# Kernel tuning notes

Hardware: AMD Instinct MI355X
Metric: run time of the kernel (lower is better)

## Reference

```python
import jax, jax.numpy as jnp
import numpy as np

EPS = 0.2        # epsilon from init_kwargs
MIN_POINTS = 10  # minPoints from init_kwargs

def setup_inputs() -> dict:
    key = jax.random.key(0)
    points = jax.random.normal(key, (16384, 3), dtype=jnp.float32)
    return {"points": points}

def _dbscan(points):
    # Faithful DBSCAN semantics of the torch module: brute-force region query
    # (dist < eps, self included since d(p,p)=0<eps), core if |neighbors| >= minPoints,
    # clusters = connected components of the eps-graph restricted to core points,
    # border points join the lowest-scan-order cluster among their core neighbors
    # (matches the sequential scan-order cluster numbering), everything else -1.
    N = points.shape[0]
    sq = jnp.sum(points * points, axis=1)                       # [N]
    # ||xi - xj||^2 via GEMM expansion (avoids the [N,N,3] diff tensor)
    d2 = sq[:, None] + sq[None, :] - 2.0 * (points @ points.T)  # [N,N]
    adj = d2 < (EPS * EPS)                                      # strict <, as in torch code
    deg = jnp.sum(adj, axis=1)
    core = deg >= MIN_POINTS                                    # [N] bool
    core_adj = adj & core[:, None] & core[None, :]              # core<->core edges

    BIG = N  # sentinel label larger than any point index
    idx = jnp.arange(N)
    lab0 = jnp.where(core, idx, BIG)

    # min-label propagation until fixed point => component root = min core index,
    # which equals the first core point of that cluster in scan order.
    def cond(state):
        _, changed = state
        return changed

    def body(state):
        lab, _ = state
        nb = jnp.min(jnp.where(core_adj, lab[None, :], BIG), axis=1)
        new = jnp.minimum(lab, nb)
        return (new, jnp.any(new != lab))

    lab, _ = jax.lax.while_loop(cond, body, (lab0, jnp.array(True)))

    # every point's root = min root among its core neighbors (core points include self)
    root = jnp.min(jnp.where(adj & core[None, :], lab[None, :], BIG), axis=1)
    reached = root < BIG  # core or border; otherwise noise

    # renumber roots to sequential cluster ids in scan order
    is_root = core & (lab == idx)
    rank = jnp.cumsum(is_root.astype(jnp.int32)) - 1            # cluster id at each root index
    cid = rank[jnp.minimum(root, N - 1)]
    labels = jnp.where(reached, cid, -1).astype(jnp.float32)
    return labels.reshape(-1, 1)

def reference(points):
    return _dbscan(points)
```

## Files before the change

### kernel.cpp

```cpp
#include <hip/hip_runtime.h>
#include <stdint.h>


#define N_PTS   16384
#define BLOCK   256
#define EPS2    0.04f
#define G       32
#define GCELLS  (G * G * G)
#define GLO     -4.5f
#define GSCALE  3.5555556f
#define NRANGE  27
#define EBLK    (NRANGE * N_PTS / BLOCK)
#define LBUF    4096
#define LB1     2048
#define ECAP    262144
#define MCAP    65536
#define SCAP    131072
#define BCAP    131072
#define HSIZE   32768
#define NCC     1024
#define CHUNK   (N_PTS / NCC)
#define BIG     N_PTS
#define ENCB    16400
#define HUGEV   (1 << 29)
#define HEMPTY  0xFFFFFFFFu


__device__ __forceinline__ float sqsum(float x, float y, float z) {
    return __fadd_rn(__fadd_rn(__fmul_rn(x, x), __fmul_rn(y, y)), __fmul_rn(z, z));
}
__device__ __forceinline__ float dist2(float px, float py, float pz, float sqi, float4 q) {
    float dot = __fmaf_rn(pz, q.z, __fmaf_rn(py, q.y, __fmul_rn(px, q.x)));
    return __fsub_rn(__fadd_rn(sqi, q.w), __fmul_rn(2.0f, dot));
}
__device__ __forceinline__ int pload(const int* p) {
    return __hip_atomic_load(p, __ATOMIC_RELAXED, __HIP_MEMORY_SCOPE_AGENT);
}
__device__ __forceinline__ uint32_t uload(const uint32_t* p) {
    return __hip_atomic_load(p, __ATOMIC_RELAXED, __HIP_MEMORY_SCOPE_AGENT);
}
__device__ __forceinline__ int cellco(float v) {
    int c = (int)floorf(__fmul_rn(__fsub_rn(v, GLO), GSCALE));
    return min(max(c, 0), G - 1);
}

__global__ void k_hist(const float* __restrict__ pts, uint32_t* __restrict__ cnts,
                       int* __restrict__ parent, uint32_t* __restrict__ htab,
                       uint32_t* __restrict__ hcnt, uint32_t* __restrict__ cellof) {
    const int p = blockIdx.x * BLOCK + threadIdx.x;
    if (blockIdx.x == 0 && threadIdx.x < 3) cnts[2 + threadIdx.x] = 0;
    parent[p] = p;
    htab[p] = HEMPTY; htab[p + N_PTS] = HEMPTY;
    float x = pts[3 * p], y = pts[3 * p + 1], z = pts[3 * p + 2];
    uint32_t c = (uint32_t)((cellco(z) * G + cellco(y)) * G + cellco(x));
    cellof[p] = c;
    atomicAdd(&hcnt[c], 1u);
}

__global__ void __launch_bounds__(1024)
k_scan(const uint32_t* __restrict__ hcnt, const uint32_t* __restrict__ cnts,
       uint32_t* __restrict__ cellstart, uint32_t* __restrict__ cursor) {
    __shared__ uint32_t wsum[16];
    const int tid = threadIdx.x, lane = tid & 63, wv = tid >> 6;
    const uint32_t B = cnts[15];
    uint32_t loc[32];
#pragma unroll
    for (int k = 0; k < 8; ++k) {
        uint4 v = ((const uint4*)hcnt)[tid * 8 + k];
        loc[4 * k + 0] = v.x - B; loc[4 * k + 1] = v.y - B;
        loc[4 * k + 2] = v.z - B; loc[4 * k + 3] = v.w - B;
    }
    uint32_t tot = 0;
#pragma unroll
    for (int k = 0; k < 32; ++k) tot += loc[k];
    uint32_t incl = tot;
#pragma unroll
    for (int d = 1; d < 64; d <<= 1) { uint32_t t2 = __shfl_up(incl, d, 64); if (lane >= d) incl += t2; }
    if (lane == 63) wsum[wv] = incl;
    __syncthreads();
    uint32_t wbase = 0;
    for (int w = 0; w < wv; ++w) wbase += wsum[w];
    uint32_t off = wbase + incl - tot;
#pragma unroll
    for (int k = 0; k < 32; ++k) {
        uint32_t c = (uint32_t)tid * 32u + (uint32_t)k;
        cellstart[c] = off; cursor[c] = off;
        off += loc[k];
    }
    if (tid == 1023) cellstart[GCELLS] = off;
}

__global__ void k_scatter(const float* __restrict__ pts, const uint32_t* __restrict__ cellof,
                          uint32_t* __restrict__ cursor, float4* __restrict__ spts,
                          int* __restrict__ sid) {
    const int p = blockIdx.x * BLOCK + threadIdx.x;
    uint32_t c = cellof[p];
    uint32_t pos = atomicAdd(&cursor[c], 1u);
    float x = pts[3 * p], y = pts[3 * p + 1], z = pts[3 * p + 2];
    spts[pos] = make_float4(x, y, z, sqsum(x, y, z));
    sid[pos] = p;
}

__global__ void k_edges_b(const float4* __restrict__ spts, const int* __restrict__ sid,
                          const uint32_t* __restrict__ cellstart,
                          uint32_t* __restrict__ edges, uint32_t* __restrict__ cnts,
                          uint32_t* __restrict__ deg) {
    const uint32_t B = cnts[15];
    const int tid = threadIdx.x;
    __shared__ uint32_t lbuf[LBUF];
    __shared__ uint32_t lcnt, lbase;
    if (tid == 0) lcnt = 0;
    __syncthreads();
    const int r = blockIdx.x >> 6;
    const int p = ((blockIdx.x & 63) << 8) + tid;
    float4 me = spts[p];
    const int ig = sid[p];
    const int cx = cellco(me.x), cy = cellco(me.y), cz = cellco(me.z);
    const int x = cx + (r % 3) - 1;
    const int y = cy + ((r / 3) % 3) - 1;
    const int z = cz + (r / 9) - 1;
    uint32_t cnt = 0;
    if ((unsigned)x < (unsigned)G && (unsigned)y < (unsigned)G && (unsigned)z < (unsigned)G) {
        const int c = (z * G + y) * G + x;
        uint32_t q = cellstart[c];
        const uint32_t qe = cellstart[c + 1];
        for (; q < qe; ++q) {
            float4 o = spts[q];
            float d2 = dist2(me.x, me.y, me.z, me.w, o);
            if (d2 < EPS2) {
                ++cnt;
                int jg = sid[q];
                if (jg < ig) {
                    uint32_t s = atomicAdd(&lcnt, 1u);
                    uint32_t pk = ((uint32_t)ig << 14) | (uint32_t)jg;
                    if (s < LBUF) lbuf[s] = pk;
                    else {
                        uint32_t pos = atomicAdd(&cnts[1], 1u) - B;
                        if (pos < ECAP) edges[pos] = pk;
                    }
                }
            }
        }
    }
    if (cnt) atomicAdd(&deg[ig], cnt);
    __syncthreads();
    if (tid == 0) {
        uint32_t n = min(lcnt, (uint32_t)LBUF);
        lcnt = n;
        lbase = atomicAdd(&cnts[1], n) - B;
    }
    __syncthreads();
    for (uint32_t t2 = tid; t2 < lcnt; t2 += BLOCK) {
        uint32_t s2 = lbase + t2;
        if (s2 < ECAP) edges[s2] = lbuf[t2];
    }
}

__global__ void k_hook0(const uint32_t* __restrict__ edges, uint32_t* __restrict__ cnts,
                        const uint32_t* __restrict__ deg, int* __restrict__ parent,
                        uint32_t* __restrict__ mbuf) {
    const uint32_t B = cnts[15];
    const int n = min((int)(uload(&cnts[1]) - B), ECAP);
    const int lane = threadIdx.x & 63;
    const uint64_t lane_lt = (1ull << lane) - 1;
    for (int e = blockIdx.x * BLOCK + threadIdx.x; e < n; e += gridDim.x * BLOCK) {
        uint32_t p = edges[e];
        int i = (int)(p >> 14), j = (int)(p & (N_PTS - 1));
        bool ci = (deg[i] - B) >= 10u;
        bool cj = (deg[j] - B) >= 10u;
        if (ci && cj) atomicMin(&parent[max(i, j)], min(i, j));
        bool mx = ci != cj;
        uint64_t m2 = __ballot(mx);
        if (m2) {
            int ldr = (int)__ffsll((unsigned long long)m2) - 1;
            uint32_t base = 0;
            if (lane == ldr) base = atomicAdd(&cnts[3], (uint32_t)__popcll(m2));
            base = __shfl(base, ldr);
            if (mx) {
                uint32_t pk = ci ? (((uint32_t)i << 14) | (uint32_t)j)
                                 : (((uint32_t)j << 14) | (uint32_t)i);
                uint32_t pos = base + (uint32_t)__popcll(m2 & lane_lt);
                if (pos < MCAP) mbuf[pos] = pk;
            }
        }
    }
}

__global__ void k_jump(int* __restrict__ parent) {
    int x = blockIdx.x * BLOCK + threadIdx.x;
    int p = pload(&parent[x]);
    if (p == x) return;
    int r = p;
    while (true) { int q = pload(&parent[r]); if (q == r) break; r = q; }
    if (r != p)
        __hip_atomic_store(&parent[x], r, __ATOMIC_RELAXED, __HIP_MEMORY_SCOPE_AGENT);
}

__global__ void k_hook1(const uint32_t* __restrict__ edges, uint32_t* __restrict__ cnts,
                        const uint32_t* __restrict__ deg, int* __restrict__ parent,
                        uint32_t* __restrict__ surv, uint32_t* __restrict__ htab) {
    const uint32_t B = cnts[15];
    const int n = min((int)(uload(&cnts[1]) - B), ECAP);
    const int tid = threadIdx.x;
    __shared__ uint32_t lbuf[LB1];
    __shared__ uint32_t lcnt, lbase;
    if (tid == 0) lcnt = 0;
    __syncthreads();
    for (int e = blockIdx.x * BLOCK + tid; e < n; e += gridDim.x * BLOCK) {
        uint32_t p = edges[e];
        int i = (int)(p >> 14), j = (int)(p & (N_PTS - 1));
        bool cc = ((deg[i] - B) >= 10u) && ((deg[j] - B) >= 10u);
        if (cc) {
            int ri = pload(&parent[i]);
            int rj = pload(&parent[j]);
            if (ri != rj) {
                int lo = min(ri, rj), hi = max(ri, rj);
                uint32_t pk = ((uint32_t)hi << 14) | (uint32_t)lo;
                uint32_t h = (pk * 2654435761u) >> 17;
                if (atomicExch(&htab[h], pk) != pk) {
                    atomicMin(&parent[hi], lo);
                    uint32_t s = atomicAdd(&lcnt, 1u);
                    if (s < LB1) lbuf[s] = pk;
                    else {
                        uint32_t pos = atomicAdd(&cnts[4], 1u);
                        if (pos < SCAP) surv[pos] = pk;
                    }
                }
            }
        }
    }
    __syncthreads();
    if (tid == 0) {
        uint32_t n2 = min(lcnt, (uint32_t)LB1);
        lcnt = n2;
        lbase = atomicAdd(&cnts[4], n2);
    }
    __syncthreads();
    for (uint32_t t2 = tid; t2 < lcnt; t2 += BLOCK) {
        uint32_t s2 = lbase + t2;
        if (s2 < SCAP) surv[s2] = lbuf[t2];
    }
}

__global__ void __launch_bounds__(NCC)
k_cc_final(const int* __restrict__ parent_g, const uint32_t* __restrict__ deg,
           const uint32_t* __restrict__ surv, uint32_t* __restrict__ cnts,
           const uint32_t* __restrict__ mbuf,
           uint32_t* __restrict__ bufA, uint32_t* __restrict__ bufB,
           float* __restrict__ out) {
    __shared__ int lpar[N_PTS];
    __shared__ int s_nout;
    __shared__ int wsum[16];
    const int tid = threadIdx.x, lane = tid & 63, wv = tid >> 6;
    const uint64_t lane_lt = (1ull << lane) - 1;
    const uint32_t B = cnts[15];

#pragma unroll
    for (int k = 0; k < CHUNK; ++k) {
        int x = k * NCC + tid;
        lpar[x] = ((deg[x] - B) >= 10u) ? pload(&parent_g[x]) : BIG;
    }
    __syncthreads();
    {
        int v[CHUNK];
#pragma unroll
        for (int k = 0; k < CHUNK; ++k) v[k] = lpar[k * NCC + tid];
        bool any = true;
        while (any) {
            any = false;
#pragma unroll
            for (int k = 0; k < CHUNK; ++k) {
                if (v[k] < BIG) {
                    int q = lpar[v[k]];
                    if (q != v[k]) { v[k] = q; any = true; }
                }
            }
        }
#pragma unroll
        for (int k = 0; k < CHUNK; ++k)
            if (v[k] < BIG) lpar[k * NCC + tid] = v[k];
    }
    __syncthreads();

    int n_in = min((int)uload(&cnts[4]), SCAP);
    const uint32_t* cur = surv;
    for (int r = 0; r < 24; ++r) {
        uint32_t* nxt = (r & 1) ? bufB : bufA;
        if (tid == 0) s_nout = 0;
        __syncthreads();
        const int n4 = (n_in + 3) & ~3;
        for (int bb = tid * 4; bb < n4; bb += NCC * 4) {
            uint4 pk4 = *(const uint4*)(cur + bb);
#pragma unroll
            for (int k = 0; k < 4; ++k) {
                uint32_t p = (k == 0) ? pk4.x : (k == 1) ? pk4.y : (k == 2) ? pk4.z : pk4.w;
                bool valid = (bb + k) < n_in;
                int ri = 0, rj = 0;
                if (valid) {
                    ri = lpar[(int)(p >> 14)];
                    rj = lpar[(int)(p & (N_PTS - 1))];
                }
                bool live = valid && (ri != rj);
                int lo = min(ri, rj), hi = max(ri, rj);
                if (live) atomicMin(&lpar[hi], lo);
                uint64_t m = __ballot(live);
                if (m) {
                    int ldr = (int)__ffsll((unsigned long long)m) - 1;
                    int base = 0;
                    if (lane == ldr) base = atomicAdd(&s_nout, (int)__popcll(m));
                    base = __shfl(base, ldr);
                    if (live) {
                        int pos = base + (int)__popcll(m & lane_lt);
                        if (pos < BCAP) nxt[pos] = ((uint32_t)hi << 14) | (uint32_t)lo;
                    }
                }
            }
        }
        __syncthreads();
        if (s_nout == 0) break;
        int v[CHUNK];
#pragma unroll
        for (int k = 0; k < CHUNK; ++k) v[k] = lpar[k * NCC + tid];
        bool any = true;
        while (any) {
            any = false;
#pragma unroll
            for (int k = 0; k < CHUNK; ++k) {
                if (v[k] < BIG) {
                    int q = lpar[v[k]];
                    if (q != v[k]) { v[k] = q; any = true; }
                }
            }
        }
#pragma unroll
        for (int k = 0; k < CHUNK; ++k)
            if (v[k] < BIG) lpar[k * NCC + tid] = v[k];
        n_in = min(s_nout, BCAP);
        cur = nxt;
    }

    const int bn = tid * CHUNK;
    int fl[CHUNK]; int s = 0;
#pragma unroll
    for (int k = 0; k < CHUNK; ++k) {
        fl[k] = (lpar[bn + k] == bn + k) ? 1 : 0;
        s += fl[k];
    }
    int incl = s;
#pragma unroll
    for (int d = 1; d < 64; d <<= 1) { int t = __shfl_up(incl, d, 64); if (lane >= d) incl += t; }
    if (lane == 63) wsum[wv] = incl;
    __syncthreads();
    int wbase = 0;
    for (int w = 0; w < wv; ++w) wbase += wsum[w];
    int c = wbase + incl - s;
#pragma unroll
    for (int k = 0; k < CHUNK; ++k)
        if (fl[k]) lpar[bn + k] = ENCB + (c++);
    __syncthreads();
#pragma unroll
    for (int k = 0; k < CHUNK; ++k) {
        int x = k * NCC + tid;
        int p = lpar[x];
        if (p < BIG) lpar[x] = lpar[p];
        else if (p == BIG) lpar[x] = HUGEV;
    }
    __syncthreads();
    int nm = min((int)uload(&cnts[3]), MCAP);
    const int nm4 = (nm + 3) & ~3;
    for (int bb = tid * 4; bb < nm4; bb += NCC * 4) {
        uint4 p4 = *(const uint4*)(mbuf + bb);
#pragma unroll
        for (int k = 0; k < 4; ++k) {
            if (bb + k < nm) {
                uint32_t p = (k == 0) ? p4.x : (k == 1) ? p4.y : (k == 2) ? p4.z : p4.w;
                int cc = (int)(p >> 14), bb2 = (int)(p & (N_PTS - 1));
                atomicMin(&lpar[bb2], lpar[cc]);
            }
        }
    }
    __syncthreads();
#pragma unroll
    for (int k = 0; k < CHUNK; ++k) {
        int x = k * NCC + tid;
        int v = lpar[x];
        out[x] = (v < HUGEV) ? (float)(v - ENCB) : -1.0f;
    }
}

extern "C" void kernel_launch(void* const* d_in, const int* in_sizes, int n_in,
                              void* d_out, int out_size, void* d_ws, size_t ws_size,
                              hipStream_t stream) {
    (void)in_sizes; (void)n_in; (void)out_size; (void)ws_size;
    const float* pts = (const float*)d_in[0];
    float* out = (float*)d_out;

    uint32_t* ub = (uint32_t*)d_ws;
    uint32_t* deg       = ub;
    int*      parent    = (int*)(ub + 16384);
    uint32_t* cnts      = ub + 32768;
    uint32_t* edges     = ub + 32832;
    uint32_t* mbuf      = ub + 294976;
    uint32_t* surv      = ub + 360512;
    uint32_t* bufA      = ub + 491584;
    uint32_t* bufB      = ub + 622656;
    uint32_t* htab      = ub + 753728;
    uint32_t* hcnt      = ub + 786496;
    uint32_t* cellstart = ub + 819264;
    uint32_t* cursor    = ub + 852048;
    uint32_t* cellof    = ub + 884816;
    int*      sid       = (int*)(ub + 901200);
    float4*   spts      = (float4*)(ub + 917584);

    dim3 blk(BLOCK);
    k_hist    <<<dim3(N_PTS / BLOCK), blk, 0, stream>>>(pts, cnts, parent, htab, hcnt, cellof);
    k_scan    <<<dim3(1), dim3(1024), 0, stream>>>(hcnt, cnts, cellstart, cursor);
    k_scatter <<<dim3(N_PTS / BLOCK), blk, 0, stream>>>(pts, cellof, cursor, spts, sid);
    k_edges_b <<<dim3(EBLK), blk, 0, stream>>>(spts, sid, cellstart, edges, cnts, deg);
    k_hook0   <<<dim3(1024), blk, 0, stream>>>(edges, cnts, deg, parent, mbuf);
    k_jump    <<<dim3(N_PTS / BLOCK), blk, 0, stream>>>(parent);
    k_hook1   <<<dim3(512), blk, 0, stream>>>(edges, cnts, deg, parent, surv, htab);
    k_cc_final<<<dim3(1), dim3(NCC), 0, stream>>>(parent, deg, surv, cnts,
                                                  mbuf, bufA, bufB, out);
}
```

Baseline: 157.6 us.

## Use half-neighbourhood cell stencil and symmetric edge emission in edge kernel

The edge-building kernel now scans only 13 forward neighbour cells plus the later points of its own cell, instead of all 27 cells. Each pair is tested once, both endpoints' degrees are incremented through an atomic on the partner, and a canonically ordered edge is emitted. Because self-pairs are no longer counted, the core threshold drops from 10 to 9. This roughly halves the distance tests, at the cost of extra global atomics on deg and more shared-buffer appends per block.

```diff
diff --git a/kernel.cpp b/kernel.cpp
--- a/kernel.cpp
+++ b/kernel.cpp
@@ -9,7 +9,7 @@
 #define GCELLS  (G * G * G)
 #define GLO     -4.5f
 #define GSCALE  3.5555556f
-#define NRANGE  27
+#define NRANGE  14
 #define EBLK    (NRANGE * N_PTS / BLOCK)
 #define LBUF    4096
 #define LB1     2048
@@ -116,28 +116,43 @@
     float4 me = spts[p];
     const int ig = sid[p];
     const int cx = cellco(me.x), cy = cellco(me.y), cz = cellco(me.z);
-    const int x = cx + (r % 3) - 1;
-    const int y = cy + ((r / 3) % 3) - 1;
-    const int z = cz + (r / 9) - 1;
+    uint32_t q = 0, qe = 0;
+    bool run = true;
+    if (r == 13) {
+        const int c = (cz * G + cy) * G + cx;
+        q = (uint32_t)p + 1u;
+        qe = cellstart[c + 1];
+        run = q < qe;
+    } else {
+        int dx, dy, dz;
+        if (r < 9)       { dz = 1; dy = r / 3 - 1; dx = r % 3 - 1; }
+        else if (r < 12) { dz = 0; dy = 1;         dx = r - 10;    }
+        else             { dz = 0; dy = 0;         dx = 1;         }
+        const int x = cx + dx, y = cy + dy, z = cz + dz;
+        run = (unsigned)x < (unsigned)G && (unsigned)y < (unsigned)G && (unsigned)z < (unsigned)G;
+        if (run) {
+            const int c = (z * G + y) * G + x;
+            q = cellstart[c];
+            qe = cellstart[c + 1];
+            run = q < qe;
+        }
+    }
     uint32_t cnt = 0;
-    if ((unsigned)x < (unsigned)G && (unsigned)y < (unsigned)G && (unsigned)z < (unsigned)G) {
-        const int c = (z * G + y) * G + x;
-        uint32_t q = cellstart[c];
-        const uint32_t qe = cellstart[c + 1];
+    if (run) {
         for (; q < qe; ++q) {
             float4 o = spts[q];
             float d2 = dist2(me.x, me.y, me.z, me.w, o);
             if (d2 < EPS2) {
                 ++cnt;
                 int jg = sid[q];
-                if (jg < ig) {
-                    uint32_t s = atomicAdd(&lcnt, 1u);
-                    uint32_t pk = ((uint32_t)ig << 14) | (uint32_t)jg;
-                    if (s < LBUF) lbuf[s] = pk;
-                    else {
-                        uint32_t pos = atomicAdd(&cnts[1], 1u) - B;
-                        if (pos < ECAP) edges[pos] = pk;
-                    }
+                atomicAdd(&deg[jg], 1u);
+                uint32_t pk = ig > jg ? (((uint32_t)ig << 14) | (uint32_t)jg)
+                                      : (((uint32_t)jg << 14) | (uint32_t)ig);
+                uint32_t s = atomicAdd(&lcnt, 1u);
+                if (s < LBUF) lbuf[s] = pk;
+                else {
+                    uint32_t pos = atomicAdd(&cnts[1], 1u) - B;
+                    if (pos < ECAP) edges[pos] = pk;
                 }
             }
         }
@@ -166,8 +181,8 @@
     for (int e = blockIdx.x * BLOCK + threadIdx.x; e < n; e += gridDim.x * BLOCK) {
         uint32_t p = edges[e];
         int i = (int)(p >> 14), j = (int)(p & (N_PTS - 1));
-        bool ci = (deg[i] - B) >= 10u;
-        bool cj = (deg[j] - B) >= 10u;
+        bool ci = (deg[i] - B) >= 9u;
+        bool cj = (deg[j] - B) >= 9u;
         if (ci && cj) atomicMin(&parent[max(i, j)], min(i, j));
         bool mx = ci != cj;
         uint64_t m2 = __ballot(mx);
@@ -209,7 +224,7 @@
     for (int e = blockIdx.x * BLOCK + tid; e < n; e += gridDim.x * BLOCK) {
         uint32_t p = edges[e];
         int i = (int)(p >> 14), j = (int)(p & (N_PTS - 1));
-        bool cc = ((deg[i] - B) >= 10u) && ((deg[j] - B) >= 10u);
+        bool cc = ((deg[i] - B) >= 9u) && ((deg[j] - B) >= 9u);
         if (cc) {
             int ri = pload(&parent[i]);
             int rj = pload(&parent[j]);
@@ -258,7 +273,7 @@
 #pragma unroll
     for (int k = 0; k < CHUNK; ++k) {
         int x = k * NCC + tid;
-        lpar[x] = ((deg[x] - B) >= 10u) ? pload(&parent_g[x]) : BIG;
+        lpar[x] = ((deg[x] - B) >= 9u) ? pload(&parent_g[x]) : BIG;
     }
     __syncthreads();
     {
```

After: 154.2 us. 2.2% less time.
